# Kernel tuning notes

Measured on AMD Instinct MI355X. Metric: run time of the kernel, lower is better.

Reference implementation:

```python
import jax, jax.numpy as jnp
import numpy as np

N = 100000        # number of nodes
E = 3200000       # number of edges (avg degree 32)
D_IN = 128
D_OUT = 128


def setup_inputs() -> dict:
    key = jax.random.key(0)
    k_x, k_src, k_dst, k_w, k_W, k_b = jax.random.split(key, 6)
    x = jax.random.normal(k_x, (N, D_IN), dtype=jnp.float32)
    edge_src = jax.random.randint(k_src, (E,), 0, N, dtype=jnp.int32)
    edge_dst = jnp.sort(jax.random.randint(k_dst, (E,), 0, N, dtype=jnp.int32))
    edge_weight = jax.random.uniform(k_w, (E,), dtype=jnp.float32)
    # Linear params, init uniform(-stdv, stdv) with stdv = 1/sqrt(in_features)
    stdv = 1.0 / np.sqrt(D_IN)
    W = jax.random.uniform(k_W, (D_IN, D_OUT), dtype=jnp.float32, minval=-stdv, maxval=stdv)
    b = jax.random.uniform(k_b, (D_OUT,), dtype=jnp.float32, minval=-stdv, maxval=stdv)
    return {"x": x, "W": W, "b": b, "edge_weight": edge_weight,
            "edge_src": edge_src, "edge_dst": edge_dst}


def reference(x, W, b, edge_weight, edge_src, edge_dst):
    # support = W(input)  -- dense projection [N, D_OUT]
    support = x @ W + b
    # output = spmm(adj, support): out[dst] += w_e * support[src]
    msgs = support[edge_src] * edge_weight[:, None]          # [E, D_OUT]
    out = jax.ops.segment_sum(msgs, edge_dst, num_segments=x.shape[0])
    return out
```

## Files before the change

kernel.cpp:

```cpp
#include <hip/hip_runtime.h>

#define D 128

typedef unsigned short u16;
typedef __attribute__((ext_vector_type(8))) short bf16x8;
typedef __attribute__((ext_vector_type(4))) float f32x4;

__device__ __forceinline__ u16 f32_to_bf16(float f) {
    unsigned u = __float_as_uint(f);
    unsigned rounding = 0x7fffu + ((u >> 16) & 1u);
    return (u16)((u + rounding) >> 16);
}

__device__ __forceinline__ float bf16_to_f32(u16 s) {
    return __uint_as_float(((unsigned)s) << 16);
}

__global__ __launch_bounds__(256) void prep_kernel(
    const float* __restrict__ W, u16* __restrict__ Wt)
{
    int idx = blockIdx.x * 256 + threadIdx.x;
    int n = idx >> 7;
    int k = idx & 127;
    Wt[idx] = f32_to_bf16(W[k * 128 + n]);
}

__global__ __launch_bounds__(256) void gemm_mfma_kernel(
    const float* __restrict__ x, const u16* __restrict__ Wt,
    const float* __restrict__ b, u16* __restrict__ sup, int N)
{
    const int lane = threadIdx.x & 63;
    const int wave = threadIdx.x >> 6;
    const int col  = lane & 15;
    const int quad = lane >> 4;
    const int row0 = blockIdx.x * 64 + wave * 16;
    const int m    = row0 + col;
    const bool mvalid = (m < N);

    f32x4 acc[8];
    #pragma unroll
    for (int nt = 0; nt < 8; ++nt) {
        float bias = b[nt * 16 + col];
        acc[nt][0] = bias; acc[nt][1] = bias;
        acc[nt][2] = bias; acc[nt][3] = bias;
    }

    const float* xrow = x + (size_t)m * D;

    #pragma unroll
    for (int ks = 0; ks < 4; ++ks) {
        const int k0 = ks * 32 + quad * 8;

        float af[8];
        if (mvalid) {
            float4 v0 = *(const float4*)(xrow + k0);
            float4 v1 = *(const float4*)(xrow + k0 + 4);
            af[0] = v0.x; af[1] = v0.y; af[2] = v0.z; af[3] = v0.w;
            af[4] = v1.x; af[5] = v1.y; af[6] = v1.z; af[7] = v1.w;
        } else {
            #pragma unroll
            for (int j = 0; j < 8; ++j) af[j] = 0.f;
        }

        bf16x8 ahi, alo;
        #pragma unroll
        for (int j = 0; j < 8; ++j) {
            u16 h = f32_to_bf16(af[j]);
            float r = af[j] - bf16_to_f32(h);
            ahi[j] = (short)h;
            alo[j] = (short)f32_to_bf16(r);
        }

        #pragma unroll
        for (int nt = 0; nt < 8; ++nt) {
            bf16x8 bfrag = *(const bf16x8*)(Wt + (size_t)(nt * 16 + col) * D + k0);
            acc[nt] = __builtin_amdgcn_mfma_f32_16x16x32_bf16(alo, bfrag, acc[nt], 0, 0, 0);
            acc[nt] = __builtin_amdgcn_mfma_f32_16x16x32_bf16(ahi, bfrag, acc[nt], 0, 0, 0);
        }
    }

    #pragma unroll
    for (int reg = 0; reg < 4; ++reg) {
        int r = row0 + quad * 4 + reg;
        if (r < N) {
            #pragma unroll
            for (int nt = 0; nt < 8; ++nt) {
                sup[(size_t)r * D + nt * 16 + col] = f32_to_bf16(acc[nt][reg]);
            }
        }
    }
}

__global__ __launch_bounds__(256) void rowptr_kernel(
    const int* __restrict__ edst, int* __restrict__ rp, int E, int N)
{
    int e = blockIdx.x * 256 + threadIdx.x;
    if (e >= E) return;
    int d = edst[e];
    int prev = (e == 0) ? -1 : edst[e - 1];
    for (int n = prev + 1; n <= d; ++n) rp[n] = e;
    if (e == E - 1) {
        for (int n = d + 1; n <= N; ++n) rp[n] = E;
    }
}

__global__ __launch_bounds__(256, 4) void spmm_kernel(
    const u16* __restrict__ sup, const float* __restrict__ ew,
    const int* __restrict__ esrc, const int* __restrict__ rp,
    float* __restrict__ out, int N)
{
    const int b    = blockIdx.x;
    const int xcd  = b & 7;
    const int half = xcd >> 2;
    const int grp  = (b >> 3) * 4 + (xcd & 3);
    const int wave = threadIdx.x >> 6;
    const int lane = threadIdx.x & 63;
    const int node = grp * 4 + wave;
    if (node >= N) return;

    const int start = rp[node];
    const int end   = rp[node + 1];

    const int eg = lane >> 3;
    const int fl = lane & 7;
    const unsigned off = (unsigned)half * 64u + (unsigned)fl * 8u;

    float acc[8];
    #pragma unroll
    for (int j = 0; j < 8; ++j) acc[j] = 0.f;

    for (int base = start; base < end; base += 64) {
        int cnt = end - base;
        if (cnt > 64) cnt = 64;

        int mi = base + lane;
        int   sv = (mi < end) ? esrc[mi] : 0;
        float wv = (mi < end) ? ew[mi]   : 0.f;

        uint4 u[8];
        float w[8];

        #pragma unroll
        for (int g = 0; g < 8; ++g) {
            if (g * 8 >= cnt) break;
            int idx = g * 8 + eg;
            int   s  = __shfl(sv, idx);
            w[g]     = __shfl(wv, idx);
            u[g] = *(const uint4*)(sup + (size_t)s * D + off);
        }

        #pragma unroll
        for (int g = 0; g < 8; ++g) {
            if (g * 8 >= cnt) break;
            unsigned d0 = u[g].x, d1 = u[g].y, d2 = u[g].z, d3 = u[g].w;
            float wg = w[g];
            acc[0] = fmaf(wg, __uint_as_float(d0 << 16),         acc[0]);
            acc[1] = fmaf(wg, __uint_as_float(d0 & 0xffff0000u), acc[1]);
            acc[2] = fmaf(wg, __uint_as_float(d1 << 16),         acc[2]);
            acc[3] = fmaf(wg, __uint_as_float(d1 & 0xffff0000u), acc[3]);
            acc[4] = fmaf(wg, __uint_as_float(d2 << 16),         acc[4]);
            acc[5] = fmaf(wg, __uint_as_float(d2 & 0xffff0000u), acc[5]);
            acc[6] = fmaf(wg, __uint_as_float(d3 << 16),         acc[6]);
            acc[7] = fmaf(wg, __uint_as_float(d3 & 0xffff0000u), acc[7]);
        }
    }

    #pragma unroll
    for (int m = 8; m <= 32; m <<= 1) {
        #pragma unroll
        for (int j = 0; j < 8; ++j) acc[j] += __shfl_xor(acc[j], m);
    }

    if (eg == 0) {
        float* dst = out + (size_t)node * D + off;
        float4 o0 = make_float4(acc[0], acc[1], acc[2], acc[3]);
        float4 o1 = make_float4(acc[4], acc[5], acc[6], acc[7]);
        *(float4*)dst       = o0;
        *(float4*)(dst + 4) = o1;
    }
}

extern "C" void kernel_launch(void* const* d_in, const int* in_sizes, int n_in,
                              void* d_out, int out_size, void* d_ws, size_t ws_size,
                              hipStream_t stream) {
    const float* x    = (const float*)d_in[0];
    const float* W    = (const float*)d_in[1];
    const float* b    = (const float*)d_in[2];
    const float* ew   = (const float*)d_in[3];
    const int*   esrc = (const int*)d_in[4];
    const int*   edst = (const int*)d_in[5];
    float* out = (float*)d_out;

    const int N = in_sizes[0] / D;
    const int E = in_sizes[3];

    u16* sup = (u16*)d_ws;
    int* rp  = (int*)((char*)d_ws + (size_t)N * D * sizeof(u16));
    u16* Wt  = (u16*)((char*)rp + ((size_t)N + 16) * sizeof(int));

    hipLaunchKernelGGL(prep_kernel, dim3(64), dim3(256), 0, stream, W, Wt);
    hipLaunchKernelGGL(gemm_mfma_kernel, dim3((N + 63) / 64), dim3(256), 0, stream,
                       x, Wt, b, sup, N);
    hipLaunchKernelGGL(rowptr_kernel, dim3((E + 255) / 256), dim3(256), 0, stream,
                       edst, rp, E, N);

    int nblk_half = (N + 3) / 4;
    int grid_spmm = ((nblk_half + 3) / 4) * 8;
    hipLaunchKernelGGL(spmm_kernel, dim3(grid_spmm), dim3(256), 0, stream,
                       sup, ew, esrc, rp, out, N);
}
```

Baseline: 264.2 us.

## Fuse W prep, GEMM and rowptr into one launch; stage W in LDS

Replaces the three separate launches (W transpose/convert, MFMA GEMM, rowptr build) with one kernel. Its first blocks build the row pointer array, and the remaining blocks each convert W to bf16 into padded shared memory before running the GEMM. The SpMM gather loop is split into two fixed halves of four edge groups with clamped indices and zeroed weights, which replaces the per-group early break. This removes two launch gaps and the global Wt round trip, but every GEMM block now re-reads and converts all of W, and the 34 KB of LDS per block may limit occupancy.

```diff
diff --git a/kernel.cpp b/kernel.cpp
--- a/kernel.cpp
+++ b/kernel.cpp
@@ -5,6 +5,8 @@
 typedef unsigned short u16;
 typedef __attribute__((ext_vector_type(8))) short bf16x8;
 typedef __attribute__((ext_vector_type(4))) float f32x4;
+
+#define WSTRIDE 136
 
 __device__ __forceinline__ u16 f32_to_bf16(float f) {
     unsigned u = __float_as_uint(f);
@@ -16,24 +18,48 @@
     return __uint_as_float(((unsigned)s) << 16);
 }
 
-__global__ __launch_bounds__(256) void prep_kernel(
-    const float* __restrict__ W, u16* __restrict__ Wt)
+__global__ __launch_bounds__(256) void gemm_rowptr_kernel(
+    const float* __restrict__ x, const float* __restrict__ W,
+    const float* __restrict__ b, u16* __restrict__ sup,
+    const int* __restrict__ edst, int* __restrict__ rp,
+    int N, int E, int G_rp)
 {
-    int idx = blockIdx.x * 256 + threadIdx.x;
-    int n = idx >> 7;
-    int k = idx & 127;
-    Wt[idx] = f32_to_bf16(W[k * 128 + n]);
-}
-
-__global__ __launch_bounds__(256) void gemm_mfma_kernel(
-    const float* __restrict__ x, const u16* __restrict__ Wt,
-    const float* __restrict__ b, u16* __restrict__ sup, int N)
-{
-    const int lane = threadIdx.x & 63;
-    const int wave = threadIdx.x >> 6;
+    __shared__ u16 wsh[128 * WSTRIDE];
+
+    if (blockIdx.x < (unsigned)G_rp) {
+        int e = blockIdx.x * 256 + threadIdx.x;
+        if (e >= E) return;
+        int d = edst[e];
+        int prev = (e == 0) ? -1 : edst[e - 1];
+        for (int n = prev + 1; n <= d; ++n) rp[n] = e;
+        if (e == E - 1) {
+            for (int n = d + 1; n <= N; ++n) rp[n] = E;
+        }
+        return;
+    }
+
+    const int gblk = blockIdx.x - G_rp;
+    const int tid  = threadIdx.x;
+
+    {
+        const int n  = tid >> 1;
+        const int kh = (tid & 1) * 64;
+        #pragma unroll 8
+        for (int i = 0; i < 32; ++i) {
+            int k = kh + i * 2;
+            float f0 = W[(size_t)k * 128 + n];
+            float f1 = W[(size_t)(k + 1) * 128 + n];
+            unsigned p = (unsigned)f32_to_bf16(f0) | ((unsigned)f32_to_bf16(f1) << 16);
+            *(unsigned*)(&wsh[n * WSTRIDE + k]) = p;
+        }
+    }
+    __syncthreads();
+
+    const int lane = tid & 63;
+    const int wave = tid >> 6;
     const int col  = lane & 15;
     const int quad = lane >> 4;
-    const int row0 = blockIdx.x * 64 + wave * 16;
+    const int row0 = gblk * 64 + wave * 16;
     const int m    = row0 + col;
     const bool mvalid = (m < N);
 
@@ -73,7 +99,7 @@
 
         #pragma unroll
         for (int nt = 0; nt < 8; ++nt) {
-            bf16x8 bfrag = *(const bf16x8*)(Wt + (size_t)(nt * 16 + col) * D + k0);
+            bf16x8 bfrag = *(const bf16x8*)(&wsh[(nt * 16 + col) * WSTRIDE + k0]);
             acc[nt] = __builtin_amdgcn_mfma_f32_16x16x32_bf16(alo, bfrag, acc[nt], 0, 0, 0);
             acc[nt] = __builtin_amdgcn_mfma_f32_16x16x32_bf16(ahi, bfrag, acc[nt], 0, 0, 0);
         }
@@ -88,19 +114,6 @@
                 sup[(size_t)r * D + nt * 16 + col] = f32_to_bf16(acc[nt][reg]);
             }
         }
-    }
-}
-
-__global__ __launch_bounds__(256) void rowptr_kernel(
-    const int* __restrict__ edst, int* __restrict__ rp, int E, int N)
-{
-    int e = blockIdx.x * 256 + threadIdx.x;
-    if (e >= E) return;
-    int d = edst[e];
-    int prev = (e == 0) ? -1 : edst[e - 1];
-    for (int n = prev + 1; n <= d; ++n) rp[n] = e;
-    if (e == E - 1) {
-        for (int n = d + 1; n <= N; ++n) rp[n] = E;
     }
 }
 
@@ -141,17 +154,28 @@
         float w[8];
 
         #pragma unroll
-        for (int g = 0; g < 8; ++g) {
-            if (g * 8 >= cnt) break;
-            int idx = g * 8 + eg;
-            int   s  = __shfl(sv, idx);
-            w[g]     = __shfl(wv, idx);
+        for (int g = 0; g < 4; ++g) {
+            int idx  = g * 8 + eg;
+            int cidx = (idx < cnt) ? idx : (cnt - 1);
+            int   s  = __shfl(sv, cidx);
+            float wt = __shfl(wv, cidx);
+            w[g] = (idx < cnt) ? wt : 0.f;
             u[g] = *(const uint4*)(sup + (size_t)s * D + off);
         }
-
-        #pragma unroll
-        for (int g = 0; g < 8; ++g) {
-            if (g * 8 >= cnt) break;
+        if (cnt > 32) {
+            #pragma unroll
+            for (int g = 4; g < 8; ++g) {
+                int idx  = g * 8 + eg;
+                int cidx = (idx < cnt) ? idx : (cnt - 1);
+                int   s  = __shfl(sv, cidx);
+                float wt = __shfl(wv, cidx);
+                w[g] = (idx < cnt) ? wt : 0.f;
+                u[g] = *(const uint4*)(sup + (size_t)s * D + off);
+            }
+        }
+
+        #pragma unroll
+        for (int g = 0; g < 4; ++g) {
             unsigned d0 = u[g].x, d1 = u[g].y, d2 = u[g].z, d3 = u[g].w;
             float wg = w[g];
             acc[0] = fmaf(wg, __uint_as_float(d0 << 16),         acc[0]);
@@ -163,6 +187,21 @@
             acc[6] = fmaf(wg, __uint_as_float(d3 << 16),         acc[6]);
             acc[7] = fmaf(wg, __uint_as_float(d3 & 0xffff0000u), acc[7]);
         }
+        if (cnt > 32) {
+            #pragma unroll
+            for (int g = 4; g < 8; ++g) {
+                unsigned d0 = u[g].x, d1 = u[g].y, d2 = u[g].z, d3 = u[g].w;
+                float wg = w[g];
+                acc[0] = fmaf(wg, __uint_as_float(d0 << 16),         acc[0]);
+                acc[1] = fmaf(wg, __uint_as_float(d0 & 0xffff0000u), acc[1]);
+                acc[2] = fmaf(wg, __uint_as_float(d1 << 16),         acc[2]);
+                acc[3] = fmaf(wg, __uint_as_float(d1 & 0xffff0000u), acc[3]);
+                acc[4] = fmaf(wg, __uint_as_float(d2 << 16),         acc[4]);
+                acc[5] = fmaf(wg, __uint_as_float(d2 & 0xffff0000u), acc[5]);
+                acc[6] = fmaf(wg, __uint_as_float(d3 << 16),         acc[6]);
+                acc[7] = fmaf(wg, __uint_as_float(d3 & 0xffff0000u), acc[7]);
+            }
+        }
     }
 
     #pragma unroll
@@ -196,13 +235,11 @@
 
     u16* sup = (u16*)d_ws;
     int* rp  = (int*)((char*)d_ws + (size_t)N * D * sizeof(u16));
-    u16* Wt  = (u16*)((char*)rp + ((size_t)N + 16) * sizeof(int));
-
-    hipLaunchKernelGGL(prep_kernel, dim3(64), dim3(256), 0, stream, W, Wt);
-    hipLaunchKernelGGL(gemm_mfma_kernel, dim3((N + 63) / 64), dim3(256), 0, stream,
-                       x, Wt, b, sup, N);
-    hipLaunchKernelGGL(rowptr_kernel, dim3((E + 255) / 256), dim3(256), 0, stream,
-                       edst, rp, E, N);
+
+    const int G_rp   = (E + 255) / 256;
+    const int G_gemm = (N + 63) / 64;
+    hipLaunchKernelGGL(gemm_rowptr_kernel, dim3(G_rp + G_gemm), dim3(256), 0, stream,
+                       x, W, b, sup, edst, rp, N, E, G_rp);
 
     int nblk_half = (N + 3) / 4;
     int grid_spmm = ((nblk_half + 3) / 4) * 8;
```

Measured after the change: 267.7 us. No clear change (+1.3%).
